# Kernel optimization log

Measured on AMD Instinct MI355X. Metric: run time of the kernel, lower is better.

The kernel has to match this reference:

```python
import jax, jax.numpy as jnp
import numpy as np

N = 131072        # total pedestrians across scenes
NUM_SEQS = 8192   # number of scenes (seq_start_end groups)
H = 128           # h_dim
E = 128           # embedding_dim (split into two halves of 64)
NK = 20           # number of motion-field regimes
PRED_LEN = 12     # decoder rollout length


def setup_inputs() -> dict:
    key = jax.random.key(0)
    ks = jax.random.split(key, 19)
    s = lambda d: 1.0 / np.sqrt(d)
    inp = {
        'state_final': jax.random.normal(ks[0], (N, H), jnp.float32) * 0.1,
        'last_pos':    jax.random.normal(ks[1], (N, 2), jnp.float32),
        'alpha0':      jax.random.uniform(ks[2], (N, NK), jnp.float32) + 1e-3,
        'fields_disp0': jax.random.normal(ks[3], (N, NK, 2), jnp.float32) * 0.1,
        'W_pos':  jax.random.normal(ks[4], (2, E // 2), jnp.float32) * s(2),
        'b_pos':  jnp.zeros((E // 2,), jnp.float32),
        'W_fld':  jax.random.normal(ks[5], (NK * 2, E // 2), jnp.float32) * s(NK * 2),
        'b_fld':  jnp.zeros((E // 2,), jnp.float32),
        'W_pool': jax.random.normal(ks[6], (H, H), jnp.float32) * s(H),
        'b_pool': jnp.zeros((H,), jnp.float32),
        'Wx':     jax.random.normal(ks[7], (E + H, 4 * H), jnp.float32) * s(E + H),
        'Wh':     jax.random.normal(ks[8], (H, 4 * H), jnp.float32) * s(H),
        'b_lstm': jnp.zeros((4 * H,), jnp.float32),
        'W_out':  jax.random.normal(ks[9], (H, 2), jnp.float32) * s(H),
        'b_out':  jnp.zeros((2,), jnp.float32),
        'field_A': jax.random.normal(ks[10], (NK, 2, 2), jnp.float32) * 0.1,
        'trans':   jax.random.normal(ks[11], (NK, NK), jnp.float32),
        'segment_ids': jnp.sort(jax.random.randint(ks[12], (N,), 0, NUM_SEQS, jnp.int32)),
        'seq_mask': jax.random.randint(ks[13], (N,), 0, 2, jnp.int32).astype(bool),
    }
    return inp


def reference(state_final, last_pos, alpha0, fields_disp0,
              W_pos, b_pos, W_fld, b_fld, W_pool, b_pool,
              Wx, Wh, b_lstm, W_out, b_out, field_A, trans,
              segment_ids, seq_mask):
    mask2 = seq_mask[:, None]                       # (N,1) valid-pedestrian mask
    alpha = alpha0 / jnp.sum(alpha0, axis=-1, keepdims=True)  # regime probs
    h, c = state_final, jnp.zeros_like(state_final)
    out0 = state_final @ W_out + b_out              # first rel displacement from encoder h
    rel = out0
    pos = last_pos + rel

    def step(carry, _):
        h, c, rel, pos, fields_disp, alpha = carry
        # masked input embedding: pos half + (displacement * probs) half
        pos_emb = rel @ W_pos + b_pos                                   # (N, E/2)
        dtp = fields_disp * alpha[:, :, None]                           # use_probs
        fld_emb = dtp.reshape(N, NK * 2) @ W_fld + b_fld                # (N, E/2)
        emb = jnp.concatenate([pos_emb, fld_emb], axis=-1)              # (N, E)
        # per-scene interaction pooling: max-pool hidden states within each sequence
        seg_max = jax.ops.segment_max(h, segment_ids, num_segments=NUM_SEQS)
        pool = seg_max[segment_ids]                                     # (N, H)
        pool_data = jax.nn.relu(pool @ W_pool + b_pool)
        # LSTM cell on concat(embedded, pool_data)
        x = jnp.concatenate([emb, pool_data], axis=-1)                  # (N, E+H)
        gates = x @ Wx + h @ Wh + b_lstm
        i, f, g, o = jnp.split(gates, 4, axis=-1)
        c_new = jax.nn.sigmoid(f) * c + jax.nn.sigmoid(i) * jnp.tanh(g)
        h_new = jax.nn.sigmoid(o) * jnp.tanh(c_new)
        h2 = jnp.where(mask2, h_new, h)
        c2 = jnp.where(mask2, c_new, c)
        out = h2 @ W_out + b_out
        rel_new = jnp.where(mask2, out, rel)
        pos_new = pos + rel_new
        # motion-fields single_prediction update (runs under no_grad in original)
        fd_prop = jax.lax.stop_gradient(jnp.einsum('nd,kde->nke', pos_new, field_A))
        al_prop = jax.lax.stop_gradient(jax.nn.softmax(alpha @ trans, axis=-1))
        fd_new = jnp.where(mask2[:, :, None], fd_prop, fields_disp)
        al_new = jnp.where(mask2, al_prop, alpha)
        return (h2, c2, rel_new, pos_new, fd_new, al_new), rel_new

    carry0 = (h, c, rel, pos, fields_disp0, alpha)
    _, outs = jax.lax.scan(step, carry0, None, length=PRED_LEN - 1)
    pred_traj_out = jnp.concatenate([out0[None], outs], axis=0)  # (PRED_LEN, N, 2)
    return pred_traj_out
```

## Files before the change

kernel.cpp:

```cpp
#include <hip/hip_runtime.h>
#include <hip/hip_bf16.h>
#include <math.h>

#define N_PTS 131072
#define NSEG  8192
#define NKK   20
#define PRED  12
#define KP    192
#define LPAD  136

typedef __hip_bfloat16 bf16;
typedef __attribute__((ext_vector_type(8))) short short8;
typedef __attribute__((ext_vector_type(2))) short short2v;
typedef __attribute__((ext_vector_type(4))) float float4v;

__device__ __forceinline__ float b2f(bf16 x){ return __bfloat162float(x); }
__device__ __forceinline__ float b2fs(short s){
  unsigned int u = ((unsigned int)(unsigned short)s)<<16;
  return __uint_as_float(u);
}
__device__ __forceinline__ unsigned short f2bu(float f){
  bf16 h = __float2bfloat16(f);
  return *reinterpret_cast<unsigned short*>(&h);
}
__device__ __forceinline__ float sigm(float x){ return 1.0f/(1.0f+__expf(-x)); }
__device__ __forceinline__ float tanh_f(float x){
  x = fminf(15.f, fmaxf(-15.f, x));
  float e = __expf(2.f*x);
  return (e-1.f)/(e+1.f);
}
__device__ __forceinline__ float ldf(const void* p, long long i, bool bf){
  return bf ? __bfloat162float(((const bf16*)p)[i]) : ((const float*)p)[i];
}
__device__ __forceinline__ int ldseg(const void* p, long long i, bool i64){
  return i64 ? (int)(((const long long*)p)[i]) : ((const int*)p)[i];
}
__device__ __forceinline__ void stf(void* p, long long i, float v, bool bf){
  if(bf) ((bf16*)p)[i] = __float2bfloat16(v);
  else   ((float*)p)[i] = v;
}

__global__ void k_probe(const unsigned short* __restrict__ wx,
                        const int* __restrict__ seg,
                        const unsigned char* __restrict__ msk,
                        int* __restrict__ flags){
  int lane = threadIdx.x & 63;
  unsigned short h1 = wx[2*lane], h2 = wx[128+2*lane];
  int e1 = (h1>>7)&255, e2 = (h2>>7)&255;
  bool p1 = (e1>=100 && e1<=132), p2 = (e2>=100 && e2<=132);
  int cnt = __popcll(__ballot(p1)) + __popcll(__ballot(p2));
  int v = seg[65536+lane];
  int zc = __popcll(__ballot((lane&1) && v==0));
  bool nz1=false, nz2=false;
  for(int i=lane;i<4096;i+=64){
    unsigned char b = msk[i];
    if((i&3)!=0 && b) nz1=true;
    if((i&7)==4 && b) nz2=true;
  }
  unsigned long long b1 = __ballot(nz1), b2 = __ballot(nz2);
  if(lane==0){
    flags[0] = (cnt>=64) ? 1 : 0;
    flags[1] = (zc>=24) ? 1 : 0;
    flags[2] = b1 ? 1 : (b2 ? 0 : 2);
  }
}

__global__ void k_conv(const unsigned char* __restrict__ mraw, const int* __restrict__ flags,
                       unsigned char* __restrict__ mask){
  int i = blockIdx.x*256+threadIdx.x;
  if(i>=N_PTS) return;
  int mode = flags[2];
  unsigned char v;
  if(mode==1)      v = mraw[i]!=0;
  else if(mode==0) v = ((const int*)mraw)[i]!=0;
  else             v = ((const long long*)mraw)[i]!=0;
  mask[i]=v;
}

__global__ void k_segstart(const void* __restrict__ seg, const int* __restrict__ flags,
                           int* __restrict__ start){
  int s = blockIdx.x*256+threadIdx.x;
  if(s>NSEG) return;
  bool i64 = flags[1]!=0;
  int lo=0, hi=N_PTS;
  while(lo<hi){ int mid=(lo+hi)>>1; if(ldseg(seg,mid,i64)<s) lo=mid+1; else hi=mid; }
  start[s]=lo;
}

__global__ void k_fold(const void* __restrict__ Wpos, const void* __restrict__ bpos,
                       const void* __restrict__ Wfld, const void* __restrict__ bfld,
                       const void* __restrict__ Wx,   const void* __restrict__ Wh,
                       const void* __restrict__ blstm, const int* __restrict__ flags,
                       short* __restrict__ wTs, float* __restrict__ bias,
                       short* __restrict__ wpoolT, const void* __restrict__ Wpool,
                       short* __restrict__ wxT2){
  int idx = blockIdx.x*256+threadIdx.x;
  bool bf = flags[0]!=0;
  if(idx < 512*KP){
    int n = idx/KP, k = idx - n*KP;
    float v;
    if(k<2){
      float a=0; for(int j=0;j<64;j++) a += ldf(Wpos,k*64+j,bf)*ldf(Wx,j*512+n,bf);
      v=a;
    } else if(k<42){
      int kk=k-2; float a=0; for(int j=0;j<64;j++) a += ldf(Wfld,kk*64+j,bf)*ldf(Wx,(64+j)*512+n,bf);
      v=a;
    } else if(k<170){
      v = ldf(Wh,(long long)(k-42)*512+n,bf);
    } else v = 0.f;
    int g = n>>7, np = n&127;
    int ntg = np>>4, lm = np&15;
    int kc = k>>5, lq = (k&31)>>3, j = k&7;
    long long addr = ((long long)((g*8+ntg)*6 + kc))*512 + lq*128 + lm*8 + j;
    ((bf16*)wTs)[addr] = __float2bfloat16(v);
  } else if(idx < 512*KP+512){
    int c = idx - 512*KP;
    float a=ldf(blstm,c,bf);
    for(int j=0;j<64;j++) a += ldf(bpos,j,bf)*ldf(Wx,j*512+c,bf) + ldf(bfld,j,bf)*ldf(Wx,(64+j)*512+c,bf);
    bias[c]=a;
  } else if(idx < 512*KP+512+128*128){
    int j = idx - (512*KP+512);
    int n = j>>7, k = j&127;
    ((bf16*)wpoolT)[j] = __float2bfloat16(ldf(Wpool,k*128+n,bf));
  } else if(idx < 512*KP+512+128*128+512*128){
    int j = idx - (512*KP+512+128*128);
    int n = j>>7, k = j&127;
    ((bf16*)wxT2)[j] = __float2bfloat16(ldf(Wx,(long long)(128+k)*512+n,bf));
  }
}

__global__ void k_init(const void* __restrict__ sf, const void* __restrict__ lastpos,
                       const void* __restrict__ alpha0, const void* __restrict__ fd0,
                       const void* __restrict__ Wout, const void* __restrict__ bout,
                       const int* __restrict__ flags,
                       short* __restrict__ Apk, float* __restrict__ c,
                       float* __restrict__ rel, float* __restrict__ pos,
                       float* __restrict__ al, void* __restrict__ traj){
  int grp = threadIdx.x>>6, lane = threadIdx.x&63;
  int p = blockIdx.x*4+grp;
  bool bf = flags[0]!=0;
  bf16* Ap = (bf16*)Apk + (long long)p*KP;
  float h0 = ldf(sf,(long long)p*128+lane,bf);
  float h1 = ldf(sf,(long long)p*128+64+lane,bf);
  Ap[42+lane]      = __float2bfloat16(h0);
  Ap[42+64+lane]   = __float2bfloat16(h1);
  c[(long long)p*128+lane]=0.f; c[(long long)p*128+64+lane]=0.f;
  float o0 = h0*ldf(Wout,lane*2,bf)   + h1*ldf(Wout,(64+lane)*2,bf);
  float o1 = h0*ldf(Wout,lane*2+1,bf) + h1*ldf(Wout,(64+lane)*2+1,bf);
  for(int m=1;m<64;m<<=1){ o0 += __shfl_xor(o0,m); o1 += __shfl_xor(o1,m); }
  o0 += ldf(bout,0,bf); o1 += ldf(bout,1,bf);
  float a = 0.f;
  if(lane<NKK) a = ldf(alpha0,(long long)p*NKK+lane,bf);
  float s = a;
  for(int m=1;m<64;m<<=1) s += __shfl_xor(s,m);
  float aln = a/s;
  if(lane<NKK) al[(long long)p*NKK+lane] = aln;
  float alq = __shfl(aln, lane>>1);
  if(lane<2*NKK) Ap[2+lane] = __float2bfloat16(ldf(fd0,(long long)p*2*NKK+lane,bf)*alq);
  if(lane<22)    Ap[170+lane] = __float2bfloat16(0.f);
  if(lane==0){
    Ap[0]=__float2bfloat16(o0); Ap[1]=__float2bfloat16(o1);
    rel[p*2]=o0; rel[p*2+1]=o1;
    pos[p*2]   = ldf(lastpos,p*2,bf)  +o0;
    pos[p*2+1] = ldf(lastpos,p*2+1,bf)+o1;
    stf(traj, (long long)p*2,   o0, bf);
    stf(traj, (long long)p*2+1, o1, bf);
  }
}

__launch_bounds__(512,2)
__global__ void s1_fused(const short* __restrict__ Apk, const int* __restrict__ start,
                         const short* __restrict__ wpoolT, const void* __restrict__ bpool,
                         const int* __restrict__ flags, const short* __restrict__ wxT2,
                         float* __restrict__ contrib){
  __shared__ short lsm[32*LPAD];
  __shared__ short lpool[32*LPAD];
  const int tid = threadIdx.x;
  const int S0  = blockIdx.x*32;

  {
    const int t64 = tid&63;
    const int wg  = tid>>6;
    #pragma unroll
    for(int pass=0; pass<4; pass++){
      const int sgl = wg + pass*8;
      const int s = S0 + sgl;
      const int a = start[s], b = start[s+1];
      float m0=-INFINITY, m1=-INFINITY;
      const short* bp0 = Apk + 42 + t64*2;
      int i=a;
      for(; i+4<=b; i+=4){
        short2v v0 = *(const short2v*)(bp0 + (long long)(i  )*KP);
        short2v v1 = *(const short2v*)(bp0 + (long long)(i+1)*KP);
        short2v v2 = *(const short2v*)(bp0 + (long long)(i+2)*KP);
        short2v v3 = *(const short2v*)(bp0 + (long long)(i+3)*KP);
        m0 = fmaxf(fmaxf(fmaxf(m0,b2fs(v0[0])),fmaxf(b2fs(v1[0]),b2fs(v2[0]))),b2fs(v3[0]));
        m1 = fmaxf(fmaxf(fmaxf(m1,b2fs(v0[1])),fmaxf(b2fs(v1[1]),b2fs(v2[1]))),b2fs(v3[1]));
      }
      for(; i<b; i++){
        short2v v = *(const short2v*)(bp0 + (long long)i*KP);
        m0 = fmaxf(m0, b2fs(v[0]));
        m1 = fmaxf(m1, b2fs(v[1]));
      }
      if(a>=b){ m0=0.f; m1=0.f; }
      unsigned int pk = (((unsigned int)f2bu(m1))<<16) | (unsigned int)f2bu(m0);
      *(unsigned int*)(&lsm[sgl*LPAD + t64*2]) = pk;
    }
  }
  __syncthreads();

  const int w  = tid>>6, l = tid&63, lm = l&15, lq = l>>4;
  const bool bf = flags[0]!=0;

  {
    float4v acc0=(float4v)(0.f), acc1=(float4v)(0.f);
    #pragma unroll
    for(int kc=0;kc<4;kc++){
      short8 b  = *(const short8*)(wpoolT + (long long)(w*16+lm)*128 + lq*8 + kc*32);
      short8 a0 = *(const short8*)(lsm + (0*16+lm)*LPAD + kc*32 + lq*8);
      short8 a1 = *(const short8*)(lsm + (1*16+lm)*LPAD + kc*32 + lq*8);
      acc0 = __builtin_amdgcn_mfma_f32_16x16x32_bf16(a0, b, acc0,0,0,0);
      acc1 = __builtin_amdgcn_mfma_f32_16x16x32_bf16(a1, b, acc1,0,0,0);
    }
    const int n = w*16+lm;
    float bv = ldf(bpool,n,bf);
    #pragma unroll
    for(int q=0;q<4;q++){
      int s0r = 0*16 + lq*4 + q;
      int s1r = 1*16 + lq*4 + q;
      lpool[s0r*LPAD+n] = (short)f2bu(fmaxf(acc0[q]+bv, 0.f));
      lpool[s1r*LPAD+n] = (short)f2bu(fmaxf(acc1[q]+bv, 0.f));
    }
  }
  __syncthreads();

  {
    float4v acc[2][4];
    #pragma unroll
    for(int mt=0;mt<2;mt++)
      #pragma unroll
      for(int j=0;j<4;j++) acc[mt][j] = (float4v)(0.f);
    #pragma unroll
    for(int kc=0;kc<4;kc++){
      short8 a0 = *(const short8*)(lpool + (0*16+lm)*LPAD + kc*32 + lq*8);
      short8 a1 = *(const short8*)(lpool + (1*16+lm)*LPAD + kc*32 + lq*8);
      short8 bb[4];
      #pragma unroll
      for(int j=0;j<4;j++)
        bb[j] = *(const short8*)(wxT2 + (long long)(w*64+j*16+lm)*128 + lq*8 + kc*32);
      #pragma unroll
      for(int j=0;j<4;j++){
        acc[0][j] = __builtin_amdgcn_mfma_f32_16x16x32_bf16(a0, bb[j], acc[0][j],0,0,0);
        acc[1][j] = __builtin_amdgcn_mfma_f32_16x16x32_bf16(a1, bb[j], acc[1][j],0,0,0);
      }
    }
    #pragma unroll
    for(int mt=0;mt<2;mt++)
      #pragma unroll
      for(int j=0;j<4;j++)
        #pragma unroll
        for(int q=0;q<4;q++){
          int s = S0 + mt*16 + lq*4 + q;
          contrib[(long long)s*512 + w*64 + j*16 + lm] = acc[mt][j][q];
        }
  }
}

__launch_bounds__(256,3)
__global__ void s2_mfma(short* __restrict__ Apk, float* __restrict__ c_st,
                        const short* __restrict__ wTs, const float* __restrict__ bias,
                        const float* __restrict__ contrib,
                        const void* __restrict__ segids, const int* __restrict__ flags,
                        const unsigned char* __restrict__ mask){
  const int tid = threadIdx.x;
  const int w   = tid>>6;
  const int l   = tid&63;
  const int lm  = l&15;
  const int lq  = l>>4;
  const int P0  = blockIdx.x*32;
  const bool i64 = flags[1]!=0;

  uchar4 mk[2];
  int sg[2][4];
  #pragma unroll
  for(int mt=0;mt<2;mt++){
    int pb = P0 + mt*16 + lq*4;
    mk[mt] = *(const uchar4*)(mask + pb);
    #pragma unroll
    for(int q=0;q<4;q++) sg[mt][q] = ldseg(segids, pb+q, i64);
  }

  float4v acc[2][4][2];
  #pragma unroll
  for(int mt=0;mt<2;mt++)
    #pragma unroll
    for(int g=0;g<4;g++)
      #pragma unroll
      for(int j=0;j<2;j++) acc[mt][g][j] = (float4v)(0.f);

  const short* ap = Apk + (long long)(P0+lm)*KP + lq*8;
  const short* bp = wTs + lq*128 + lm*8;

  #pragma unroll
  for(int kc=0;kc<6;kc++){
    short8 a0 = *(const short8*)(ap + 0*16*KP + kc*32);
    short8 a1 = *(const short8*)(ap + 1*16*KP + kc*32);
    short8 b[4][2];
    #pragma unroll
    for(int g=0;g<4;g++)
      #pragma unroll
      for(int j=0;j<2;j++)
        b[g][j] = *(const short8*)(bp + ((long long)((g*8 + w*2 + j)*6 + kc))*512);
    #pragma unroll
    for(int g=0;g<4;g++)
      #pragma unroll
      for(int j=0;j<2;j++){
        acc[0][g][j] = __builtin_amdgcn_mfma_f32_16x16x32_bf16(a0, b[g][j], acc[0][g][j],0,0,0);
        acc[1][g][j] = __builtin_amdgcn_mfma_f32_16x16x32_bf16(a1, b[g][j], acc[1][g][j],0,0,0);
      }
  }

  __syncthreads();

  float bi[4][2];
  #pragma unroll
  for(int g=0;g<4;g++)
    #pragma unroll
    for(int j=0;j<2;j++)
      bi[g][j] = bias[g*128 + w*32 + j*16 + lm];

  #pragma unroll
  for(int mt=0;mt<2;mt++){
    #pragma unroll
    for(int q=0;q<4;q++){
      unsigned char mq = (q==0)?mk[mt].x:(q==1)?mk[mt].y:(q==2)?mk[mt].z:mk[mt].w;
      if(!mq) continue;
      int p = P0 + mt*16 + lq*4 + q;
      const float* cb = contrib + (long long)sg[mt][q]*512;
      float* crow = c_st + (long long)p*128;
      bf16* hrow = (bf16*)Apk + (long long)p*KP + 42;
      #pragma unroll
      for(int j=0;j<2;j++){
        int d = w*32 + j*16 + lm;
        float gi = acc[mt][0][j][q] + bi[0][j] + cb[      d];
        float gf = acc[mt][1][j][q] + bi[1][j] + cb[128 + d];
        float gg = acc[mt][2][j][q] + bi[2][j] + cb[256 + d];
        float go = acc[mt][3][j][q] + bi[3][j] + cb[384 + d];
        float co = crow[d];
        float cn = sigm(gf)*co + sigm(gi)*tanh_f(gg);
        float hn = sigm(go)*tanh_f(cn);
        crow[d] = cn;
        hrow[d] = __float2bfloat16(hn);
      }
    }
  }
}

__global__ void s3_post(const short* __restrict__ Apk_c, short* __restrict__ Apk,
                        float* __restrict__ rel, float* __restrict__ pos, float* __restrict__ al,
                        const void* __restrict__ Wout, const void* __restrict__ bout,
                        const void* __restrict__ fieldA, const void* __restrict__ trans,
                        const int* __restrict__ flags,
                        const unsigned char* __restrict__ mask, void* __restrict__ traj, int t){
  int grp = threadIdx.x>>6, lane = threadIdx.x&63;
  int p = blockIdx.x*4+grp;
  bool bf = flags[0]!=0;
  const bf16* hrow = (const bf16*)Apk_c + (long long)p*KP + 42;
  float h0 = b2f(hrow[lane]), h1 = b2f(hrow[64+lane]);
  float o0 = h0*ldf(Wout,lane*2,bf)   + h1*ldf(Wout,(64+lane)*2,bf);
  float o1 = h0*ldf(Wout,lane*2+1,bf) + h1*ldf(Wout,(64+lane)*2+1,bf);
  for(int m=1;m<64;m<<=1){ o0 += __shfl_xor(o0,m); o1 += __shfl_xor(o1,m); }
  o0 += ldf(bout,0,bf); o1 += ldf(bout,1,bf);
  bool msk = mask[p]!=0;
  float r0 = rel[p*2], r1 = rel[p*2+1];
  if(msk){ r0=o0; r1=o1; }
  float pn0 = pos[p*2]+r0, pn1 = pos[p*2+1]+r1;
  float a_l = (lane<NKK)? al[(long long)p*NKK+lane] : 0.f;
  float ad = -INFINITY;
  if(lane<NKK){
    float a2=0.f;
    #pragma unroll
    for(int i=0;i<NKK;i++) a2 += __shfl(a_l,i)*ldf(trans,i*NKK+lane,bf);
    ad = a2;
  }
  float mx = ad;
  for(int m=1;m<64;m<<=1) mx = fmaxf(mx, __shfl_xor(mx,m));
  float e = (lane<NKK)? __expf(ad-mx) : 0.f;
  float se = e;
  for(int m=1;m<64;m<<=1) se += __shfl_xor(se,m);
  float alp = e/se;
  if(msk && lane<NKK) al[(long long)p*NKK+lane] = alp;
  float alq = __shfl(alp, lane>>1);
  if(msk && lane<2*NKK){
    int kk=lane>>1, ee=lane&1;
    float fp = pn0*ldf(fieldA,kk*4+ee,bf) + pn1*ldf(fieldA,kk*4+2+ee,bf);
    ((bf16*)Apk)[(long long)p*KP+2+lane] = __float2bfloat16(fp*alq);
  }
  if(lane==0){
    if(msk){
      ((bf16*)Apk)[(long long)p*KP+0] = __float2bfloat16(r0);
      ((bf16*)Apk)[(long long)p*KP+1] = __float2bfloat16(r1);
    }
    rel[p*2]=r0; rel[p*2+1]=r1;
    pos[p*2]=pn0; pos[p*2+1]=pn1;
    long long base = (long long)t*N_PTS*2 + (long long)p*2;
    stf(traj, base,   r0, bf);
    stf(traj, base+1, r1, bf);
  }
}

extern "C" void kernel_launch(void* const* d_in, const int* in_sizes, int n_in,
                              void* d_out, int out_size, void* d_ws, size_t ws_size,
                              hipStream_t stream){
  const void* sf      = d_in[0];
  const void* lastpos = d_in[1];
  const void* alpha0  = d_in[2];
  const void* fd0     = d_in[3];
  const void* Wpos    = d_in[4];
  const void* bpos    = d_in[5];
  const void* Wfld    = d_in[6];
  const void* bfld    = d_in[7];
  const void* Wpool   = d_in[8];
  const void* bpool   = d_in[9];
  const void* Wx      = d_in[10];
  const void* Wh      = d_in[11];
  const void* blstm   = d_in[12];
  const void* Wout    = d_in[13];
  const void* bout    = d_in[14];
  const void* fieldA  = d_in[15];
  const void* trans   = d_in[16];
  const void* segids  = d_in[17];
  const unsigned char* maskraw = (const unsigned char*)d_in[18];

  char* ws = (char*)d_ws;
  size_t o = 0;
  auto alc = [&](size_t b){ size_t r=o; o=(o+b+255)&~(size_t)255; return r; };
  short* Apk       = (short*)(ws+alc((size_t)N_PTS*KP*2));
  float* c_st      = (float*)(ws+alc((size_t)N_PTS*128*4));
  float* rel       = (float*)(ws+alc((size_t)N_PTS*2*4));
  float* pos       = (float*)(ws+alc((size_t)N_PTS*2*4));
  float* al        = (float*)(ws+alc((size_t)N_PTS*20*4));
  int*   segst     = (int*)  (ws+alc((size_t)(NSEG+1)*4));
  float* contrib   = (float*)(ws+alc((size_t)NSEG*512*4));
  short* wTs       = (short*)(ws+alc((size_t)512*KP*2));
  float* bias      = (float*)(ws+alc((size_t)512*4));
  short* wpoolT    = (short*)(ws+alc((size_t)128*128*2));
  short* wxT2      = (short*)(ws+alc((size_t)512*128*2));
  unsigned char* mask = (unsigned char*)(ws+alc((size_t)N_PTS));
  int*   flags     = (int*)  (ws+alc(64));

  k_probe<<<1,64,0,stream>>>((const unsigned short*)Wx, (const int*)segids, maskraw, flags);
  k_conv<<<512,256,0,stream>>>(maskraw, flags, mask);
  k_segstart<<<33,256,0,stream>>>(segids, flags, segst);
  k_fold<<<706,256,0,stream>>>(Wpos,bpos,Wfld,bfld,Wx,Wh,blstm,flags,wTs,bias,wpoolT,Wpool,wxT2);
  k_init<<<32768,256,0,stream>>>(sf,lastpos,alpha0,fd0,Wout,bout,flags,Apk,c_st,rel,pos,al,d_out);

  for(int t=1;t<PRED;t++){
    s1_fused<<<NSEG/32,512,0,stream>>>(Apk, segst, wpoolT, bpool, flags, wxT2, contrib);
    s2_mfma<<<N_PTS/32,256,0,stream>>>(Apk, c_st, wTs, bias, contrib, segids, flags, mask);
    s3_post<<<N_PTS/4,256,0,stream>>>(Apk, Apk, rel, pos, al, Wout, bout, fieldA, trans, flags, mask, d_out, t);
  }
}
```

Baseline: 2.339 ms.

## Fuse post-step update with next step's pooling into one concurrent kernel

Adds a combined kernel whose first 256 blocks do the segment max-pool and pool/Wx GEMMs for the next step, while the remaining blocks do the per-pedestrian output, position and regime update for the current step. The two halves touch disjoint columns of the packed activation buffer and both only read the hidden state written by the preceding LSTM kernel, so they can run side by side. This removes one launch and one serialization point per step and lets the small pooling grid overlap with the memory-bound post-processing. In exchange, the post-processing work now runs under 512-thread blocks with a launch bound of two blocks per CU, which may reduce its occupancy.

```diff
diff --git a/kernel.cpp b/kernel.cpp
--- a/kernel.cpp
+++ b/kernel.cpp
@@ -409,6 +409,157 @@
   }
 }
 
+__launch_bounds__(512,2)
+__global__ void s3s1(short* __restrict__ Apk,
+                     float* __restrict__ rel, float* __restrict__ pos, float* __restrict__ al,
+                     const void* __restrict__ Wout, const void* __restrict__ bout,
+                     const void* __restrict__ fieldA, const void* __restrict__ trans,
+                     const int* __restrict__ flags,
+                     const unsigned char* __restrict__ mask, void* __restrict__ traj, int t,
+                     const int* __restrict__ start,
+                     const short* __restrict__ wpoolT, const void* __restrict__ bpool,
+                     const short* __restrict__ wxT2, float* __restrict__ contrib){
+  __shared__ short lsm[32*LPAD];
+  __shared__ short lpool[32*LPAD];
+  const int tid = threadIdx.x;
+
+  if(blockIdx.x < 256){
+    const int S0  = blockIdx.x*32;
+    {
+      const int t64 = tid&63;
+      const int wg  = tid>>6;
+      #pragma unroll
+      for(int pass=0; pass<4; pass++){
+        const int sgl = wg + pass*8;
+        const int s = S0 + sgl;
+        const int a = start[s], b = start[s+1];
+        float m0=-INFINITY, m1=-INFINITY;
+        const short* bp0 = Apk + 42 + t64*2;
+        int i=a;
+        for(; i+4<=b; i+=4){
+          short2v v0 = *(const short2v*)(bp0 + (long long)(i  )*KP);
+          short2v v1 = *(const short2v*)(bp0 + (long long)(i+1)*KP);
+          short2v v2 = *(const short2v*)(bp0 + (long long)(i+2)*KP);
+          short2v v3 = *(const short2v*)(bp0 + (long long)(i+3)*KP);
+          m0 = fmaxf(fmaxf(fmaxf(m0,b2fs(v0[0])),fmaxf(b2fs(v1[0]),b2fs(v2[0]))),b2fs(v3[0]));
+          m1 = fmaxf(fmaxf(fmaxf(m1,b2fs(v0[1])),fmaxf(b2fs(v1[1]),b2fs(v2[1]))),b2fs(v3[1]));
+        }
+        for(; i<b; i++){
+          short2v v = *(const short2v*)(bp0 + (long long)i*KP);
+          m0 = fmaxf(m0, b2fs(v[0]));
+          m1 = fmaxf(m1, b2fs(v[1]));
+        }
+        if(a>=b){ m0=0.f; m1=0.f; }
+        unsigned int pk = (((unsigned int)f2bu(m1))<<16) | (unsigned int)f2bu(m0);
+        *(unsigned int*)(&lsm[sgl*LPAD + t64*2]) = pk;
+      }
+    }
+    __syncthreads();
+
+    const int w  = tid>>6, l = tid&63, lm = l&15, lq = l>>4;
+    const bool bf = flags[0]!=0;
+
+    {
+      float4v acc0=(float4v)(0.f), acc1=(float4v)(0.f);
+      #pragma unroll
+      for(int kc=0;kc<4;kc++){
+        short8 b  = *(const short8*)(wpoolT + (long long)(w*16+lm)*128 + lq*8 + kc*32);
+        short8 a0 = *(const short8*)(lsm + (0*16+lm)*LPAD + kc*32 + lq*8);
+        short8 a1 = *(const short8*)(lsm + (1*16+lm)*LPAD + kc*32 + lq*8);
+        acc0 = __builtin_amdgcn_mfma_f32_16x16x32_bf16(a0, b, acc0,0,0,0);
+        acc1 = __builtin_amdgcn_mfma_f32_16x16x32_bf16(a1, b, acc1,0,0,0);
+      }
+      const int n = w*16+lm;
+      float bv = ldf(bpool,n,bf);
+      #pragma unroll
+      for(int q=0;q<4;q++){
+        int s0r = 0*16 + lq*4 + q;
+        int s1r = 1*16 + lq*4 + q;
+        lpool[s0r*LPAD+n] = (short)f2bu(fmaxf(acc0[q]+bv, 0.f));
+        lpool[s1r*LPAD+n] = (short)f2bu(fmaxf(acc1[q]+bv, 0.f));
+      }
+    }
+    __syncthreads();
+
+    {
+      float4v acc[2][4];
+      #pragma unroll
+      for(int mt=0;mt<2;mt++)
+        #pragma unroll
+        for(int j=0;j<4;j++) acc[mt][j] = (float4v)(0.f);
+      #pragma unroll
+      for(int kc=0;kc<4;kc++){
+        short8 a0 = *(const short8*)(lpool + (0*16+lm)*LPAD + kc*32 + lq*8);
+        short8 a1 = *(const short8*)(lpool + (1*16+lm)*LPAD + kc*32 + lq*8);
+        short8 bb[4];
+        #pragma unroll
+        for(int j=0;j<4;j++)
+          bb[j] = *(const short8*)(wxT2 + (long long)(w*64+j*16+lm)*128 + lq*8 + kc*32);
+        #pragma unroll
+        for(int j=0;j<4;j++){
+          acc[0][j] = __builtin_amdgcn_mfma_f32_16x16x32_bf16(a0, bb[j], acc[0][j],0,0,0);
+          acc[1][j] = __builtin_amdgcn_mfma_f32_16x16x32_bf16(a1, bb[j], acc[1][j],0,0,0);
+        }
+      }
+      #pragma unroll
+      for(int mt=0;mt<2;mt++)
+        #pragma unroll
+        for(int j=0;j<4;j++)
+          #pragma unroll
+          for(int q=0;q<4;q++){
+            int s = S0 + mt*16 + lq*4 + q;
+            contrib[(long long)s*512 + w*64 + j*16 + lm] = acc[mt][j][q];
+          }
+    }
+  } else {
+    int grp = tid>>6, lane = tid&63;
+    int p = (blockIdx.x-256)*8+grp;
+    bool bf = flags[0]!=0;
+    const bf16* hrow = (const bf16*)Apk + (long long)p*KP + 42;
+    float h0 = b2f(hrow[lane]), h1 = b2f(hrow[64+lane]);
+    float o0 = h0*ldf(Wout,lane*2,bf)   + h1*ldf(Wout,(64+lane)*2,bf);
+    float o1 = h0*ldf(Wout,lane*2+1,bf) + h1*ldf(Wout,(64+lane)*2+1,bf);
+    for(int m=1;m<64;m<<=1){ o0 += __shfl_xor(o0,m); o1 += __shfl_xor(o1,m); }
+    o0 += ldf(bout,0,bf); o1 += ldf(bout,1,bf);
+    bool msk = mask[p]!=0;
+    float r0 = rel[p*2], r1 = rel[p*2+1];
+    if(msk){ r0=o0; r1=o1; }
+    float pn0 = pos[p*2]+r0, pn1 = pos[p*2+1]+r1;
+    float a_l = (lane<NKK)? al[(long long)p*NKK+lane] : 0.f;
+    float ad = -INFINITY;
+    if(lane<NKK){
+      float a2=0.f;
+      #pragma unroll
+      for(int i=0;i<NKK;i++) a2 += __shfl(a_l,i)*ldf(trans,i*NKK+lane,bf);
+      ad = a2;
+    }
+    float mx = ad;
+    for(int m=1;m<64;m<<=1) mx = fmaxf(mx, __shfl_xor(mx,m));
+    float e = (lane<NKK)? __expf(ad-mx) : 0.f;
+    float se = e;
+    for(int m=1;m<64;m<<=1) se += __shfl_xor(se,m);
+    float alp = e/se;
+    if(msk && lane<NKK) al[(long long)p*NKK+lane] = alp;
+    float alq = __shfl(alp, lane>>1);
+    if(msk && lane<2*NKK){
+      int kk=lane>>1, ee=lane&1;
+      float fp = pn0*ldf(fieldA,kk*4+ee,bf) + pn1*ldf(fieldA,kk*4+2+ee,bf);
+      ((bf16*)Apk)[(long long)p*KP+2+lane] = __float2bfloat16(fp*alq);
+    }
+    if(lane==0){
+      if(msk){
+        ((bf16*)Apk)[(long long)p*KP+0] = __float2bfloat16(r0);
+        ((bf16*)Apk)[(long long)p*KP+1] = __float2bfloat16(r1);
+      }
+      rel[p*2]=r0; rel[p*2+1]=r1;
+      pos[p*2]=pn0; pos[p*2+1]=pn1;
+      long long base = (long long)t*N_PTS*2 + (long long)p*2;
+      stf(traj, base,   r0, bf);
+      stf(traj, base+1, r1, bf);
+    }
+  }
+}
+
 extern "C" void kernel_launch(void* const* d_in, const int* in_sizes, int n_in,
                               void* d_out, int out_size, void* d_ws, size_t ws_size,
                               hipStream_t stream){
@@ -455,9 +606,16 @@
   k_fold<<<706,256,0,stream>>>(Wpos,bpos,Wfld,bfld,Wx,Wh,blstm,flags,wTs,bias,wpoolT,Wpool,wxT2);
   k_init<<<32768,256,0,stream>>>(sf,lastpos,alpha0,fd0,Wout,bout,flags,Apk,c_st,rel,pos,al,d_out);
 
+  s1_fused<<<NSEG/32,512,0,stream>>>(Apk, segst, wpoolT, bpool, flags, wxT2, contrib);
   for(int t=1;t<PRED;t++){
-    s1_fused<<<NSEG/32,512,0,stream>>>(Apk, segst, wpoolT, bpool, flags, wxT2, contrib);
     s2_mfma<<<N_PTS/32,256,0,stream>>>(Apk, c_st, wTs, bias, contrib, segids, flags, mask);
-    s3_post<<<N_PTS/4,256,0,stream>>>(Apk, Apk, rel, pos, al, Wout, bout, fieldA, trans, flags, mask, d_out, t);
-  }
-}
+    if(t < PRED-1){
+      s3s1<<<256 + N_PTS/8, 512, 0, stream>>>(Apk, rel, pos, al, Wout, bout, fieldA, trans,
+                                              flags, mask, d_out, t,
+                                              segst, wpoolT, bpool, wxT2, contrib);
+    } else {
+      s3_post<<<N_PTS/4,256,0,stream>>>(Apk, Apk, rel, pos, al, Wout, bout, fieldA, trans,
+                                        flags, mask, d_out, t);
+    }
+  }
+}
```

After: 2.394 ms. 2.3% more time.
